# Performance work log

Measured on AMD Instinct MI355X. Metric: run time of the kernel, lower is better.

The kernel has to match this reference:

```python
import jax, jax.numpy as jnp
import numpy as np
from jax.scipy.linalg import solve_triangular

EPS = 2e-05  # module eps (original only adds it on Cholesky failure)
NUM_LABELS = 8


def setup_inputs() -> dict:
    key = jax.random.key(0)
    k1, k2, k3, k4 = jax.random.split(key, 4)
    B, N, H, W = 1, 256, 512, 512
    return {
        "content_feat": jax.random.normal(k1, (B, N, H, W), dtype=jnp.float32),
        "style_feat": jax.random.normal(k2, (B, N, H, W), dtype=jnp.float32),
        "content_seg": jax.random.randint(k3, (H, W), 0, NUM_LABELS, dtype=jnp.int32),
        "style_seg": jax.random.randint(k4, (H, W), 0, NUM_LABELS, dtype=jnp.int32),
        "num_labels": NUM_LABELS,
    }


def _cwct(c, s, seg_c, seg_s, num_labels):
    # c, s: (N, M) flattened features; seg_*: (M,) int labels
    N = c.shape[0]
    eye = jnp.eye(N, dtype=c.dtype)
    target = c
    for l in range(num_labels):  # fixed small label count
        mc = (seg_c == l)  # (Mc,) content mask
        ms = (seg_s == l)
        nc = mc.sum().astype(c.dtype)
        ns = ms.sum().astype(c.dtype)
        nc1 = jnp.maximum(nc, 1.0)
        ns1 = jnp.maximum(ns, 1.0)
        # masked mean + centered (zeros outside mask)
        mean_c = (c * mc).sum(-1) / nc1
        xc = (c - mean_c[:, None]) * mc  # (N, M)
        cov_c = (xc @ xc.T) / jnp.maximum(nc1 - 1.0, 1.0)  # (N, N)
        Lc = jnp.linalg.cholesky(cov_c)
        inv_Lc = solve_triangular(Lc, eye, lower=True)
        white = inv_Lc @ xc
        # style stats + coloring
        mean_s = (s * ms).sum(-1) / ns1
        xs = (s - mean_s[:, None]) * ms
        cov_s = (xs @ xs.T) / jnp.maximum(ns1 - 1.0, 1.0)
        Ls = jnp.linalg.cholesky(cov_s)
        colored = Ls @ white + mean_s[:, None]
        # label validity: >10 pixels each side, count ratio < 100
        valid = (nc > 10) & (ns > 10) & (nc < 100.0 * ns) & (ns < 100.0 * nc)
        target = jnp.where(mc[None, :] & valid, colored, target)
    return target


def reference(content_feat, style_feat, content_seg, style_seg, num_labels):
    B, N, cH, cW = content_feat.shape  # B == 1 (original code only supports B=1)
    c = content_feat.reshape(N, cH * cW)
    s = style_feat.reshape(N, -1)
    out = _cwct(c, s, content_seg.reshape(-1), style_seg.reshape(-1), num_labels)
    return out.reshape(B, N, cH, cW)
```

## Files before the change

kernel.cpp:

```cpp
#include <hip/hip_runtime.h>

#define NCH   256
#define M_PIX 262144
#define MPAD  266240
#define LDA   40

typedef short bf16x8 __attribute__((ext_vector_type(8)));
typedef float f32x4  __attribute__((ext_vector_type(4)));

__device__ __forceinline__ unsigned short f2bf(float f) {
  union { float f; unsigned u; } v; v.f = f;
  unsigned r = v.u + 0x7FFFu + ((v.u >> 16) & 1u);
  return (unsigned short)(r >> 16);
}
__device__ __forceinline__ float bf2f(unsigned short h) {
  union { unsigned u; float f; } v; v.u = ((unsigned)h) << 16;
  return v.f;
}

__global__ __launch_bounds__(256) void k_hist(const int* __restrict__ seg_c,
                                              const int* __restrict__ seg_s,
                                              int* __restrict__ hist) {
  __shared__ int h[16];
  int t = threadIdx.x;
  if (t < 16) h[t] = 0;
  __syncthreads();
  int p0 = blockIdx.x * 2048 + t * 8;
#pragma unroll
  for (int e = 0; e < 8; ++e) {
    atomicAdd(&h[seg_c[p0 + e] & 7], 1);
    atomicAdd(&h[8 + (seg_s[p0 + e] & 7)], 1);
  }
  __syncthreads();
  if (t < 8) hist[blockIdx.x * 8 + t] = h[t];
  else if (t < 16) hist[1024 + blockIdx.x * 8 + (t - 8)] = h[t];
}

__global__ __launch_bounds__(256) void k_scan(const int* __restrict__ hist,
                                              int* __restrict__ base,
                                              int* __restrict__ off,
                                              int* __restrict__ cnt,
                                              int* __restrict__ valid) {
  __shared__ int lh[2048];
  __shared__ int tot[16];
  __shared__ int loff[2][9];
  int t = threadIdx.x;
  for (int i = t; i < 2048; i += 256) lh[i] = hist[i];
  __syncthreads();
  if (t < 16) {
    int s = t >> 3, l = t & 7, acc = 0;
    for (int b = 0; b < 128; ++b) acc += lh[s * 1024 + b * 8 + l];
    tot[t] = acc;
  }
  __syncthreads();
  if (t < 2) {
    int run = 0;
    for (int l = 0; l < 8; ++l) {
      loff[t][l] = run;
      run = (run + tot[t * 8 + l] + 511) & ~511;
    }
    loff[t][8] = run;
    for (int l = 0; l < 9; ++l) off[t * 9 + l] = loff[t][l];
    for (int l = 0; l < 8; ++l) cnt[t * 8 + l] = tot[t * 8 + l];
  }
  __syncthreads();
  if (t < 8) {
    long nc = tot[t], ns = tot[8 + t];
    valid[t] = (nc > 10 && ns > 10 && nc < 100 * ns && ns < 100 * nc) ? 1 : 0;
  }
  if (t < 16) {
    int s = t >> 3, l = t & 7;
    int run = loff[s][l];
    for (int b = 0; b < 128; ++b) {
      base[s * 1024 + b * 8 + l] = run;
      run += lh[s * 1024 + b * 8 + l];
    }
  }
}

__global__ __launch_bounds__(256) void k_rank(const int* __restrict__ seg_c,
                                              const int* __restrict__ seg_s,
                                              const int* __restrict__ base,
                                              int* __restrict__ dst) {
  __shared__ int sc[8 * 272];
  __shared__ int rb[256 * 8];
  __shared__ int bb[8];
  int t = threadIdx.x;
  for (int s = 0; s < 2; ++s) {
    const int* seg = s ? seg_s : seg_c;
    const int* bas = base + s * 1024 + blockIdx.x * 8;
    int* dd = dst + (size_t)s * M_PIX;
    int p0 = blockIdx.x * 2048 + t * 8;
    unsigned pk2 = 0, cpk = 0;
#pragma unroll
    for (int e = 0; e < 8; ++e) {
      int lb = seg[p0 + e] & 7;
      pk2 |= (unsigned)lb << (3 * e);
      cpk += 1u << (4 * lb);
    }
#pragma unroll
    for (int lq = 0; lq < 8; ++lq) sc[lq * 272 + t] = (int)((cpk >> (4 * lq)) & 15u);
    if (t < 8) bb[t] = bas[t];
    __syncthreads();
    for (int d = 1; d < 256; d <<= 1) {
      int v[8];
#pragma unroll
      for (int lq = 0; lq < 8; ++lq)
        v[lq] = sc[lq * 272 + t] + ((t >= d) ? sc[lq * 272 + t - d] : 0);
      __syncthreads();
#pragma unroll
      for (int lq = 0; lq < 8; ++lq) sc[lq * 272 + t] = v[lq];
      __syncthreads();
    }
#pragma unroll
    for (int lq = 0; lq < 8; ++lq)
      rb[t * 8 + lq] = bb[lq] + sc[lq * 272 + t] - (int)((cpk >> (4 * lq)) & 15u);
#pragma unroll
    for (int e = 0; e < 8; ++e) {
      int lb = (int)((pk2 >> (3 * e)) & 7u);
      int dpos = rb[t * 8 + lb]++;
      dd[p0 + e] = dpos;
    }
    __syncthreads();
  }
}

__global__ __launch_bounds__(256) void k_padzero(unsigned short* __restrict__ P,
                                                 const int* __restrict__ off,
                                                 const int* __restrict__ cnt) {
  int l = blockIdx.x;
  int c0, c1;
  if (l < 8) { c0 = off[l] + cnt[l]; c1 = off[l + 1]; }
  else       { c0 = off[8];          c1 = MPAD; }
  int w = c1 - c0;
  if (w <= 0) return;
  for (int r = 0; r < 256; ++r)
    for (int cc = threadIdx.x; cc < w; cc += 256)
      P[(size_t)r * MPAD + c0 + cc] = 0;
}

__global__ __launch_bounds__(256) void k_pack(const float* __restrict__ feat,
                                              const int* __restrict__ seg,
                                              const int* __restrict__ dst,
                                              const int* __restrict__ base,
                                              unsigned short* __restrict__ P) {
  int b = blockIdx.x, g = blockIdx.y, t = threadIdx.x;
  int p0 = b * 2048;
  __shared__ unsigned short buf[8][2048];
  __shared__ int h[8], lbase[9], gbase[8];
  if (t < 8) { h[t] = 0; gbase[t] = base[b * 8 + t]; }
  __syncthreads();
  int lbr[2][4], slotr[2][4], gd[8];
#pragma unroll
  for (int j = 0; j < 2; ++j) {
    int4 sg = *(const int4*)&seg[p0 + j * 1024 + t * 4];
    lbr[j][0] = sg.x & 7; lbr[j][1] = sg.y & 7;
    lbr[j][2] = sg.z & 7; lbr[j][3] = sg.w & 7;
#pragma unroll
    for (int e = 0; e < 4; ++e) atomicAdd(&h[lbr[j][e]], 1);
  }
  __syncthreads();
  if (t == 0) {
    int run = 0;
    for (int l = 0; l < 8; ++l) { lbase[l] = run; run += h[l]; }
    lbase[8] = run;
  }
  __syncthreads();
#pragma unroll
  for (int j = 0; j < 2; ++j) {
    int4 dv = *(const int4*)&dst[p0 + j * 1024 + t * 4];
    slotr[j][0] = lbase[lbr[j][0]] + (dv.x - gbase[lbr[j][0]]);
    slotr[j][1] = lbase[lbr[j][1]] + (dv.y - gbase[lbr[j][1]]);
    slotr[j][2] = lbase[lbr[j][2]] + (dv.z - gbase[lbr[j][2]]);
    slotr[j][3] = lbase[lbr[j][3]] + (dv.w - gbase[lbr[j][3]]);
  }
#pragma unroll
  for (int i = 0; i < 8; ++i) {
    int q = i * 256 + t;
    int l = 0;
    while (l < 7 && q >= lbase[l + 1]) ++l;
    gd[i] = gbase[l] + q - lbase[l];
  }
  int n0 = g * 32;
#pragma unroll 1
  for (int cp = 0; cp < 4; ++cp) {
#pragma unroll
    for (int c = 0; c < 8; ++c) {
      const float* fp = &feat[(size_t)(n0 + cp * 8 + c) * M_PIX + p0];
      float4 v0 = *(const float4*)&fp[t * 4];
      float4 v1 = *(const float4*)&fp[1024 + t * 4];
      buf[c][slotr[0][0]] = f2bf(v0.x); buf[c][slotr[0][1]] = f2bf(v0.y);
      buf[c][slotr[0][2]] = f2bf(v0.z); buf[c][slotr[0][3]] = f2bf(v0.w);
      buf[c][slotr[1][0]] = f2bf(v1.x); buf[c][slotr[1][1]] = f2bf(v1.y);
      buf[c][slotr[1][2]] = f2bf(v1.z); buf[c][slotr[1][3]] = f2bf(v1.w);
    }
    __syncthreads();
#pragma unroll
    for (int c = 0; c < 8; ++c) {
      unsigned short* pp = &P[(size_t)(n0 + cp * 8 + c) * MPAD];
#pragma unroll
      for (int i = 0; i < 8; ++i)
        pp[gd[i]] = buf[c][i * 256 + t];
    }
    __syncthreads();
  }
}

__global__ __launch_bounds__(256) void k_unpack(const unsigned short* __restrict__ P,
                                                const int* __restrict__ seg,
                                                const int* __restrict__ dst,
                                                const int* __restrict__ base,
                                                float* __restrict__ out) {
  int b = blockIdx.x, g = blockIdx.y, t = threadIdx.x;
  int p0 = b * 2048;
  __shared__ unsigned short buf[8][2048];
  __shared__ int h[8], lbase[9], gbase[8];
  if (t < 8) { h[t] = 0; gbase[t] = base[b * 8 + t]; }
  __syncthreads();
  int lbr[2][4], slotr[2][4], gd[8];
#pragma unroll
  for (int j = 0; j < 2; ++j) {
    int4 sg = *(const int4*)&seg[p0 + j * 1024 + t * 4];
    lbr[j][0] = sg.x & 7; lbr[j][1] = sg.y & 7;
    lbr[j][2] = sg.z & 7; lbr[j][3] = sg.w & 7;
#pragma unroll
    for (int e = 0; e < 4; ++e) atomicAdd(&h[lbr[j][e]], 1);
  }
  __syncthreads();
  if (t == 0) {
    int run = 0;
    for (int l = 0; l < 8; ++l) { lbase[l] = run; run += h[l]; }
    lbase[8] = run;
  }
  __syncthreads();
#pragma unroll
  for (int j = 0; j < 2; ++j) {
    int4 dv = *(const int4*)&dst[p0 + j * 1024 + t * 4];
    slotr[j][0] = lbase[lbr[j][0]] + (dv.x - gbase[lbr[j][0]]);
    slotr[j][1] = lbase[lbr[j][1]] + (dv.y - gbase[lbr[j][1]]);
    slotr[j][2] = lbase[lbr[j][2]] + (dv.z - gbase[lbr[j][2]]);
    slotr[j][3] = lbase[lbr[j][3]] + (dv.w - gbase[lbr[j][3]]);
  }
#pragma unroll
  for (int i = 0; i < 8; ++i) {
    int q = i * 256 + t;
    int l = 0;
    while (l < 7 && q >= lbase[l + 1]) ++l;
    gd[i] = gbase[l] + q - lbase[l];
  }
  int n0 = g * 32;
#pragma unroll 1
  for (int cp = 0; cp < 4; ++cp) {
#pragma unroll
    for (int c = 0; c < 8; ++c) {
      const unsigned short* pp = &P[(size_t)(n0 + cp * 8 + c) * MPAD];
#pragma unroll
      for (int i = 0; i < 8; ++i)
        buf[c][i * 256 + t] = pp[gd[i]];
    }
    __syncthreads();
#pragma unroll
    for (int c = 0; c < 8; ++c) {
      float* op = &out[(size_t)(n0 + cp * 8 + c) * M_PIX + p0];
      float4 v0, v1;
      v0.x = bf2f(buf[c][slotr[0][0]]); v0.y = bf2f(buf[c][slotr[0][1]]);
      v0.z = bf2f(buf[c][slotr[0][2]]); v0.w = bf2f(buf[c][slotr[0][3]]);
      v1.x = bf2f(buf[c][slotr[1][0]]); v1.y = bf2f(buf[c][slotr[1][1]]);
      v1.z = bf2f(buf[c][slotr[1][2]]); v1.w = bf2f(buf[c][slotr[1][3]]);
      *(float4*)&op[t * 4] = v0;
      *(float4*)&op[1024 + t * 4] = v1;
    }
    __syncthreads();
  }
}

__global__ __launch_bounds__(512) void k_gram(const unsigned short* __restrict__ P,
                                              const int* __restrict__ off,
                                              float* __restrict__ G,
                                              float* __restrict__ sum) {
  int l = blockIdx.y;
  long o0 = off[l], o1 = off[l + 1];
  long k0 = o0 + (long)blockIdx.x * 1024;
  if (k0 >= o1) return;
  long rem = o1 - k0;
  int ks = rem > 1024 ? 1024 : (int)rem;

  __shared__ unsigned short Sb[256 * LDA];
  int t = threadIdx.x, wave = t >> 6, lane = t & 63;
  int wr = (wave < 2) ? wave * 64 : 128 + (wave & 1) * 64;
  int wc = (wave >= 4) ? 128 : 0;
  bool wact = (wave < 6);

  f32x4 acc[4][8] = {};
  float rsum = 0.0f;

  for (int kk = 0; kk < ks; kk += 32) {
#pragma unroll
    for (int it = 0; it < 2; ++it) {
      int slot = t + it * 512;
      int rr = slot >> 2, gg = slot & 3;
      *(uint4*)&Sb[rr * LDA + gg * 8] =
          *(const uint4*)&P[(size_t)rr * MPAD + (size_t)(k0 + kk) + gg * 8];
    }
    __syncthreads();
    if (t < 256) {
#pragma unroll
      for (int e = 0; e < 16; ++e) {
        unsigned v = *(const unsigned*)&Sb[t * LDA + e * 2];
        rsum += bf2f((unsigned short)(v & 0xFFFFu)) + bf2f((unsigned short)(v >> 16));
      }
    }
    if (wact) {
      bf16x8 bfr[8];
#pragma unroll
      for (int fj = 0; fj < 8; ++fj)
        bfr[fj] = *(const bf16x8*)&Sb[(wc + fj * 16 + (lane & 15)) * LDA + (lane >> 4) * 8];
#pragma unroll
      for (int fi = 0; fi < 4; ++fi) {
        bf16x8 afr = *(const bf16x8*)&Sb[(wr + fi * 16 + (lane & 15)) * LDA + (lane >> 4) * 8];
#pragma unroll
        for (int fj = 0; fj < 8; ++fj)
          acc[fi][fj] = __builtin_amdgcn_mfma_f32_16x16x32_bf16(afr, bfr[fj], acc[fi][fj], 0, 0, 0);
      }
    }
    __syncthreads();
  }
  float* Gl = G + ((size_t)l << 16);
  if (wact) {
#pragma unroll
    for (int fi = 0; fi < 4; ++fi)
#pragma unroll
      for (int fj = 0; fj < 8; ++fj) {
        int cc = wc + fj * 16 + (lane & 15);
#pragma unroll
        for (int rg = 0; rg < 4; ++rg) {
          int rr2 = wr + fi * 16 + (lane >> 4) * 4 + rg;
          atomicAdd(&Gl[rr2 * 256 + cc], acc[fi][fj][rg]);
        }
      }
  }
  if (t < 256) atomicAdd(&sum[l * 256 + t], rsum);
}

__global__ __launch_bounds__(256) void k_cov(float* __restrict__ G,
                                             const float* __restrict__ sum,
                                             const int* __restrict__ cnt,
                                             float* __restrict__ means,
                                             float* __restrict__ bacc) {
  int bid = blockIdx.x;
  float* A = G + ((size_t)bid << 16);
  int t = threadIdx.x;
  __shared__ float mu[256];
  float fc = (float)cnt[bid];
  float m = sum[bid * 256 + t] / fmaxf(fc, 1.0f);
  mu[t] = m;
  means[bid * 256 + t] = m;
  if (bid >= 8) bacc[(bid - 8) * 256 + t] = m;
  __syncthreads();
  float rdiv = 1.0f / fmaxf(fmaxf(fc, 1.0f) - 1.0f, 1.0f);
  float mt = mu[t];
  for (int i = t; i < 256; ++i) {
    float g = A[i * 256 + t];
    A[t * 256 + i] = (g - fc * mu[i] * mt) * rdiv;
  }
}

__global__ __launch_bounds__(256) void k_panel64(float* __restrict__ G,
                                                 float* __restrict__ Wg, int pb) {
  float* LT = G + ((size_t)blockIdx.x << 16);
  int t = threadIdx.x;
  int jb = pb * 64;
  int nT = 224 - jb;
  __shared__ float W1[32 * 36];
  __shared__ float W2[32 * 36];
  __shared__ float Cb[32][33];
  __shared__ float Db[32][33];

  if (t < 64) {
    int l32 = t & 31;
    float x[32];
#pragma unroll
    for (int k = 0; k < 32; ++k)
      x[k] = (k <= l32) ? LT[(size_t)(jb + k) * 256 + jb + l32] : 0.0f;
#pragma unroll
    for (int j = 0; j < 32; ++j) {
      float dj = __shfl(x[j], j, 64);
      float rd = 1.0f / sqrtf(dj);
      float lj = x[j] * rd;
      x[j] = lj;
#pragma unroll
      for (int k = j + 1; k < 32; ++k)
        x[k] -= lj * __shfl(lj, k, 64);
    }
    if (t < 32) {
#pragma unroll
      for (int k = 0; k < 32; ++k)
        if (k <= l32) LT[(size_t)(jb + k) * 256 + jb + l32] = x[k];
    }
    float w[32];
#pragma unroll
    for (int k = 0; k < 32; ++k) w[k] = 0.0f;
#pragma unroll
    for (int i2 = 0; i2 < 32; ++i2) {
      float s = (i2 == l32) ? 1.0f : 0.0f;
#pragma unroll
      for (int k = 0; k < 32; ++k)
        if (k < i2) s -= __shfl(x[k], i2, 64) * w[k];
      float wv = s / __shfl(x[i2], i2, 64);
      w[i2] = (i2 >= l32) ? wv : 0.0f;
    }
    if (t < 32) {
      float* Wgp = Wg + (((size_t)blockIdx.x * 8 + 2 * pb) << 10);
#pragma unroll
      for (int i2 = 0; i2 < 32; ++i2)
        if (i2 >= l32) { W1[i2 * 36 + l32] = w[i2]; Wgp[i2 * 32 + l32] = w[i2]; }
    }
  }
  __syncthreads();

  float xx[32], bb[32];
  if (t < nT) {
    int row = jb + 32 + t;
    float a[32];
#pragma unroll
    for (int k = 0; k < 32; ++k) a[k] = LT[(size_t)(jb + k) * 256 + row];
#pragma unroll
    for (int j = 0; j < 32; ++j) {
      float s = 0.0f;
#pragma unroll
      for (int k = 0; k < 32; ++k)
        if (k <= j) s += a[k] * W1[j * 36 + k];
      xx[j] = s;
      LT[(size_t)(jb + j) * 256 + row] = s;
    }
    if (t < 32) {
#pragma unroll
      for (int j = 0; j < 32; ++j) Cb[t][j] = xx[j];
    }
  }
  __syncthreads();

  if (t < nT) {
    int row = jb + 32 + t;
#pragma unroll
    for (int c = 0; c < 32; ++c) {
      float s = LT[(size_t)(jb + 32 + c) * 256 + row];
#pragma unroll
      for (int k = 0; k < 32; ++k) s -= xx[k] * Cb[c][k];
      bb[c] = s;
    }
    if (t < 32) {
#pragma unroll
      for (int c = 0; c < 32; ++c) Db[t][c] = bb[c];
    }
  }
  __syncthreads();

  if (t < 64) {
    int l32 = t & 31;
    float x[32];
#pragma unroll
    for (int k = 0; k < 32; ++k) x[k] = (k <= l32) ? Db[l32][k] : 0.0f;
#pragma unroll
    for (int j = 0; j < 32; ++j) {
      float dj = __shfl(x[j], j, 64);
      float rd = 1.0f / sqrtf(dj);
      float lj = x[j] * rd;
      x[j] = lj;
#pragma unroll
      for (int k = j + 1; k < 32; ++k)
        x[k] -= lj * __shfl(lj, k, 64);
    }
    if (t < 32) {
#pragma unroll
      for (int k = 0; k < 32; ++k)
        if (k <= l32) LT[(size_t)(jb + 32 + k) * 256 + jb + 32 + l32] = x[k];
    }
    float w[32];
#pragma unroll
    for (int k = 0; k < 32; ++k) w[k] = 0.0f;
#pragma unroll
    for (int i2 = 0; i2 < 32; ++i2) {
      float s = (i2 == l32) ? 1.0f : 0.0f;
#pragma unroll
      for (int k = 0; k < 32; ++k)
        if (k < i2) s -= __shfl(x[k], i2, 64) * w[k];
      float wv = s / __shfl(x[i2], i2, 64);
      w[i2] = (i2 >= l32) ? wv : 0.0f;
    }
    if (t < 32) {
      float* Wgp = Wg + (((size_t)blockIdx.x * 8 + 2 * pb + 1) << 10);
#pragma unroll
      for (int i2 = 0; i2 < 32; ++i2)
        if (i2 >= l32) { W2[i2 * 36 + l32] = w[i2]; Wgp[i2 * 32 + l32] = w[i2]; }
    }
  }
  __syncthreads();

  if (t >= 32 && t < nT) {
    int row = jb + 32 + t;
#pragma unroll
    for (int j = 0; j < 32; ++j) {
      float s = 0.0f;
#pragma unroll
      for (int k = 0; k < 32; ++k)
        if (k <= j) s += bb[k] * W2[j * 36 + k];
      LT[(size_t)(jb + 32 + j) * 256 + row] = s;
    }
  }
}

__global__ __launch_bounds__(256) void k_trail64(float* __restrict__ G, int pb) {
  int jb = pb * 64;
  int H2 = 192 - jb;
  int nts2 = H2 >> 6;
  int y = blockIdx.y;
  if (y >= (nts2 * (nts2 + 1)) >> 1) return;
  int ti = 0;
  while ((((ti + 1) * (ti + 2)) >> 1) <= y) ++ti;
  int tj = y - ((ti * (ti + 1)) >> 1);
  float* LT = G + ((size_t)blockIdx.x << 16);
  int i0 = jb + 64 + ti * 64, j0 = jb + 64 + tj * 64;

  __shared__ float Li[64][64];
  __shared__ float Lj[64][64];
  int t = threadIdx.x;
  for (int idx = t; idx < 4096; idx += 256) {
    int k = idx >> 6, r = idx & 63;
    Li[k][r] = LT[(size_t)(jb + k) * 256 + i0 + r];
    Lj[k][r] = LT[(size_t)(jb + k) * 256 + j0 + r];
  }
  __syncthreads();

  int tx = t & 15, ty = t >> 4;
  float acc[4][4] = {};
#pragma unroll 4
  for (int k = 0; k < 64; ++k) {
    float4 a = *(const float4*)&Li[k][ty * 4];
    float4 b = *(const float4*)&Lj[k][tx * 4];
    acc[0][0] += a.x * b.x; acc[0][1] += a.x * b.y; acc[0][2] += a.x * b.z; acc[0][3] += a.x * b.w;
    acc[1][0] += a.y * b.x; acc[1][1] += a.y * b.y; acc[1][2] += a.y * b.z; acc[1][3] += a.y * b.w;
    acc[2][0] += a.z * b.x; acc[2][1] += a.z * b.y; acc[2][2] += a.z * b.z; acc[2][3] += a.z * b.w;
    acc[3][0] += a.w * b.x; acc[3][1] += a.w * b.y; acc[3][2] += a.w * b.z; acc[3][3] += a.w * b.w;
  }
#pragma unroll
  for (int jj = 0; jj < 4; ++jj) {
    int j = j0 + tx * 4 + jj;
    float* col = &LT[(size_t)j * 256 + i0 + ty * 4];
#pragma unroll
    for (int ii = 0; ii < 4; ++ii) {
      int i = i0 + ty * 4 + ii;
      if (i >= j) col[ii] -= acc[ii][jj];
    }
  }
}

__global__ __launch_bounds__(256) void k_vlevel32w(const float* __restrict__ G,
                                                   const float* __restrict__ Wg,
                                                   float* __restrict__ Vinv) {
  int l = blockIdx.x >> 2, pair = blockIdx.x & 3;
  const float* LT = G + ((size_t)l << 16);
  float* V = Vinv + ((size_t)l << 16);
  const float* W1g = Wg + (((size_t)l * 8 + 2 * pair) << 10);
  const float* W2g = Wg + (((size_t)l * 8 + 2 * pair + 1) << 10);
  int d = pair * 64;
  int t = threadIdx.x;
  __shared__ float A[32][33];
  __shared__ float B[32][33];
  __shared__ float C[32][33];
  for (int idx = t; idx < 1024; idx += 256) {
    int i = idx >> 5, j = idx & 31;
    A[i][j] = LT[(size_t)(d + j) * 256 + d + 32 + i];
    float w1 = (i >= j) ? W1g[idx] : 0.0f;
    B[i][j] = w1;
    V[(size_t)(d + i) * 256 + d + j] = w1;
  }
  __syncthreads();
  for (int idx = t; idx < 1024; idx += 256) {
    int i = idx >> 5, j = idx & 31;
    float s = 0.0f;
#pragma unroll
    for (int k = 0; k < 32; ++k) s += A[i][k] * B[k][j];
    C[i][j] = s;
  }
  __syncthreads();
  for (int idx = t; idx < 1024; idx += 256) {
    int i = idx >> 5, j = idx & 31;
    float w2 = (i >= j) ? W2g[idx] : 0.0f;
    B[i][j] = w2;
    V[(size_t)(d + 32 + i) * 256 + d + 32 + j] = w2;
  }
  __syncthreads();
  for (int idx = t; idx < 1024; idx += 256) {
    int i = idx >> 5, j = idx & 31;
    float s = 0.0f;
#pragma unroll
    for (int k = 0; k < 32; ++k) s += B[i][k] * C[k][j];
    V[(size_t)(d + 32 + i) * 256 + d + j] = -s;
  }
}

template <int N>
__global__ __launch_bounds__(512) void k_vlevel(const float* __restrict__ G,
                                                float* __restrict__ Vinv) {
  constexpr int NP = 256 / (2 * N);
  constexpr int RPT = N / 32;
  constexpr int CPT = N / 16;
  int unit = blockIdx.x;
  int l = unit / NP, pair = unit % NP;
  const float* LT = G + ((size_t)l << 16);
  float* V = Vinv + ((size_t)l << 16);
  int d = pair * 2 * N;
  int t = threadIdx.x;
  int cg = t & 15, rg = t >> 4;
  int r0 = rg * RPT, c0 = cg * CPT;

  __shared__ float Abuf[N][N + 4];
  __shared__ float Bbuf[N][N + 4];

  for (int idx = t; idx < N * N; idx += 512) {
    int k = idx / N, r = idx % N;
    Abuf[r][k] = LT[(size_t)(d + k) * 256 + d + N + r];
  }
  for (int idx = t; idx < N * N; idx += 512) {
    int k = idx / N, c = idx % N;
    Bbuf[k][c] = V[(size_t)(d + k) * 256 + d + c];
  }
  __syncthreads();

  float acc[RPT][CPT];
#pragma unroll
  for (int i = 0; i < RPT; ++i)
#pragma unroll
    for (int j = 0; j < CPT; ++j) acc[i][j] = 0.0f;
  for (int k = 0; k < N; ++k) {
    float av[RPT];
#pragma unroll
    for (int i = 0; i < RPT; ++i) av[i] = Abuf[r0 + i][k];
#pragma unroll
    for (int j = 0; j < CPT; ++j) {
      float bv = Bbuf[k][c0 + j];
#pragma unroll
      for (int i = 0; i < RPT; ++i) acc[i][j] += av[i] * bv;
    }
  }
  __syncthreads();
#pragma unroll
  for (int i = 0; i < RPT; ++i)
#pragma unroll
    for (int j = 0; j < CPT; ++j) Abuf[r0 + i][c0 + j] = acc[i][j];
  for (int idx = t; idx < N * N; idx += 512) {
    int r = idx / N, k = idx % N;
    Bbuf[r][k] = V[(size_t)(d + N + r) * 256 + d + N + k];
  }
  __syncthreads();

#pragma unroll
  for (int i = 0; i < RPT; ++i)
#pragma unroll
    for (int j = 0; j < CPT; ++j) acc[i][j] = 0.0f;
  for (int k = 0; k < N; ++k) {
    float av[RPT];
#pragma unroll
    for (int i = 0; i < RPT; ++i) av[i] = Bbuf[r0 + i][k];
#pragma unroll
    for (int j = 0; j < CPT; ++j) {
      float bv = Abuf[k][c0 + j];
#pragma unroll
      for (int i = 0; i < RPT; ++i) acc[i][j] += av[i] * bv;
    }
  }
#pragma unroll
  for (int i = 0; i < RPT; ++i)
#pragma unroll
    for (int j = 0; j < CPT; ++j)
      V[(size_t)(d + N + r0 + i) * 256 + d + c0 + j] = -acc[i][j];
}

__global__ __launch_bounds__(256) void k_tgemm(const float* __restrict__ G,
                                               const float* __restrict__ Vinv,
                                               const float* __restrict__ means,
                                               const int* __restrict__ valid,
                                               unsigned short* __restrict__ Tb,
                                               float* __restrict__ bacc) {
  int l = blockIdx.y;
  int ti = blockIdx.x >> 2, tj = blockIdx.x & 3;
  unsigned short* Tbl = Tb + ((size_t)l << 16);
  int i0 = ti * 64, j0 = tj * 64;
  int t = threadIdx.x;
  if (!valid[l]) {
    if (tj == 0 && t < 64) bacc[l * 256 + i0 + t] = 0.0f;
    for (int idx = t; idx < 4096; idx += 256) {
      int i = idx >> 6, j = idx & 63;
      Tbl[(size_t)(i0 + i) * 256 + j0 + j] = f2bf((i0 + i) == (j0 + j) ? 1.0f : 0.0f);
    }
    return;
  }
  if (tj > ti) {
    for (int idx = t; idx < 4096; idx += 256) {
      int i = idx >> 6, j = idx & 63;
      Tbl[(size_t)(i0 + i) * 256 + j0 + j] = 0;
    }
    return;
  }
  const float* LTs = G + ((size_t)(8 + l) << 16);
  const float* V = Vinv + ((size_t)l << 16);

  __shared__ float As[64][260];
  __shared__ __align__(16) float Bs[256][68];

  for (int idx = t; idx < 64 * 256; idx += 256) {
    int k = idx >> 6, i = idx & 63;
    As[i][k] = (i0 + i >= k) ? LTs[(size_t)k * 256 + i0 + i] : 0.0f;
  }
  for (int idx = t; idx < 64 * 256; idx += 256) {
    int k = idx >> 6, j = idx & 63;
    Bs[k][j] = V[(size_t)k * 256 + j0 + j];
  }
  __syncthreads();

  int tx = t & 15, ty = t >> 4;
  float acc[4][4] = {};
  int klo = j0, khi = i0 + 64;
  for (int k = klo; k < khi; ++k) {
    float a0 = As[ty * 4 + 0][k], a1 = As[ty * 4 + 1][k];
    float a2 = As[ty * 4 + 2][k], a3 = As[ty * 4 + 3][k];
    float4 b = *(const float4*)&Bs[k][tx * 4];
    acc[0][0] += a0 * b.x; acc[0][1] += a0 * b.y; acc[0][2] += a0 * b.z; acc[0][3] += a0 * b.w;
    acc[1][0] += a1 * b.x; acc[1][1] += a1 * b.y; acc[1][2] += a1 * b.z; acc[1][3] += a1 * b.w;
    acc[2][0] += a2 * b.x; acc[2][1] += a2 * b.y; acc[2][2] += a2 * b.z; acc[2][3] += a2 * b.w;
    acc[3][0] += a3 * b.x; acc[3][1] += a3 * b.y; acc[3][2] += a3 * b.z; acc[3][3] += a3 * b.w;
  }
  float mc[4];
#pragma unroll
  for (int cc = 0; cc < 4; ++cc) mc[cc] = means[l * 256 + j0 + tx * 4 + cc];
#pragma unroll
  for (int rr = 0; rr < 4; ++rr) {
    int i = i0 + ty * 4 + rr;
    float partial = 0.0f;
#pragma unroll
    for (int cc = 0; cc < 4; ++cc) {
      Tbl[(size_t)i * 256 + j0 + tx * 4 + cc] = f2bf(acc[rr][cc]);
      partial += acc[rr][cc] * mc[cc];
    }
    atomicAdd(&bacc[l * 256 + i], -partial);
  }
}

__global__ __launch_bounds__(512) void k_outgemm(unsigned short* __restrict__ P,
                                                 const unsigned short* __restrict__ Tb,
                                                 const float* __restrict__ bvec,
                                                 const int* __restrict__ off) {
  long px0 = (long)blockIdx.x * 256;
  if (px0 >= off[8]) return;
  int l = 0;
  while (l < 7 && px0 >= off[l + 1]) ++l;
  const unsigned short* Tl = Tb + ((size_t)l << 16);

  __shared__ unsigned short As[256 * LDA];
  __shared__ unsigned short Bs[256 * LDA];
  __shared__ float bsh[256];

  int t = threadIdx.x, wave = t >> 6, lane = t & 63;
  int wrow = (wave & 3) * 64;
  int ph = wave >> 2;
  if (t < 256) bsh[t] = bvec[l * 256 + t];

  f32x4 acc[4][8] = {};

  for (int kk = 0; kk < 256; kk += 32) {
#pragma unroll
    for (int it = 0; it < 2; ++it) {
      int slot = t + it * 512;
      int rr = slot >> 2, gg = slot & 3;
      *(uint4*)&As[rr * LDA + gg * 8] = *(const uint4*)&Tl[rr * 256 + kk + gg * 8];
    }
#pragma unroll
    for (int it = 0; it < 2; ++it) {
      int slot = t + it * 512;
      int pg = slot & 31, kr = slot >> 5;
      uint4 v = *(const uint4*)&P[(size_t)(kk + kr) * MPAD + px0 + pg * 8];
      const unsigned short* vs = (const unsigned short*)&v;
      int krs = kr ^ ((pg & 3) << 3);
#pragma unroll
      for (int e = 0; e < 8; ++e) Bs[(pg * 8 + e) * LDA + krs] = vs[e];
    }
    __syncthreads();
    if (kk < wrow + 64) {
      bf16x8 bfr[8];
#pragma unroll
      for (int fj = 0; fj < 8; ++fj) {
        int px = ph * 128 + fj * 16 + (lane & 15);
        int gs = (lane >> 4) ^ ((px >> 3) & 3);
        bfr[fj] = *(const bf16x8*)&Bs[px * LDA + gs * 8];
      }
#pragma unroll
      for (int fi = 0; fi < 4; ++fi) {
        if (wrow + fi * 16 + 15 >= kk) {
          bf16x8 afr = *(const bf16x8*)&As[(wrow + fi * 16 + (lane & 15)) * LDA + (lane >> 4) * 8];
#pragma unroll
          for (int fj = 0; fj < 8; ++fj)
            acc[fi][fj] = __builtin_amdgcn_mfma_f32_16x16x32_bf16(afr, bfr[fj], acc[fi][fj], 0, 0, 0);
        }
      }
    }
    __syncthreads();
  }
#pragma unroll
  for (int fi = 0; fi < 4; ++fi)
#pragma unroll
    for (int fj = 0; fj < 8; ++fj) {
      long p = px0 + ph * 128 + fj * 16 + (lane & 15);
#pragma unroll
      for (int rg = 0; rg < 4; ++rg) {
        int rr = wrow + fi * 16 + (lane >> 4) * 4 + rg;
        float v = acc[fi][fj][rg] + bsh[rr];
        P[(size_t)rr * MPAD + p] = f2bf(v);
      }
    }
}

extern "C" void kernel_launch(void* const* d_in, const int* in_sizes, int n_in,
                              void* d_out, int out_size, void* d_ws, size_t ws_size,
                              hipStream_t stream) {
  const float* cfeat = (const float*)d_in[0];
  const float* sfeat = (const float*)d_in[1];
  const int* seg_c   = (const int*)d_in[2];
  const int* seg_s   = (const int*)d_in[3];

  char* ws = (char*)d_ws;
  size_t o = 0;
  auto take = [&](size_t b) { size_t r = o; o += (b + 255) & ~(size_t)255; return r; };

  unsigned short* P  = (unsigned short*)(ws + take((size_t)NCH * MPAD * 2));
  size_t zero_b = o;
  float* G           = (float*)(ws + take((size_t)2 * 8 * 65536 * 4));
  float* Vinv        = (float*)(ws + take((size_t)8 * 65536 * 4));
  float* sum         = (float*)(ws + take((size_t)2 * 8 * 256 * 4));
  float* bacc        = (float*)(ws + take((size_t)8 * 256 * 4));
  int*   hist        = (int*)(ws + take((size_t)2 * 128 * 8 * 4));
  size_t zero_e = o;
  unsigned short* Tb = (unsigned short*)(ws + take((size_t)8 * 65536 * 2));
  float* Wg          = (float*)(ws + take((size_t)16 * 8 * 1024 * 4));
  int*   dst         = (int*)(ws + take((size_t)2 * M_PIX * 4));
  float* means       = (float*)(ws + take((size_t)2 * 8 * 256 * 4));
  int*   base        = (int*)(ws + take((size_t)2 * 128 * 8 * 4));
  int*   off         = (int*)(ws + take((size_t)2 * 9 * 4));
  int*   cnt         = (int*)(ws + take((size_t)2 * 8 * 4));
  int*   valid       = (int*)(ws + take((size_t)8 * 4));
  (void)ws_size; (void)n_in; (void)in_sizes; (void)out_size;

  hipMemsetAsync(ws + zero_b, 0, zero_e - zero_b, stream);

  k_hist<<<dim3(128), dim3(256), 0, stream>>>(seg_c, seg_s, hist);
  k_scan<<<dim3(1), dim3(256), 0, stream>>>(hist, base, off, cnt, valid);
  k_rank<<<dim3(128), dim3(256), 0, stream>>>(seg_c, seg_s, base, dst);

  for (int s = 1; s >= 0; --s) {
    const float* feat = s ? sfeat : cfeat;
    const int* seg = s ? seg_s : seg_c;
    k_padzero<<<dim3(9), dim3(256), 0, stream>>>(P, off + s * 9, cnt + s * 8);
    k_pack<<<dim3(128, 8), dim3(256), 0, stream>>>(feat, seg, dst + (size_t)s * M_PIX,
                                                   base + s * 1024, P);
    k_gram<<<dim3(260, 8), dim3(512), 0, stream>>>(P, off + s * 9, G + (size_t)s * 8 * 65536,
                                                   sum + (size_t)s * 8 * 256);
  }

  k_cov<<<dim3(16), dim3(256), 0, stream>>>(G, sum, cnt, means, bacc);
  for (int pb = 0; pb < 4; ++pb) {
    k_panel64<<<dim3(16), dim3(256), 0, stream>>>(G, Wg, pb);
    if (pb < 3) {
      int nts2 = (192 - 64 * pb) >> 6;
      k_trail64<<<dim3(16, (nts2 * (nts2 + 1)) >> 1), dim3(256), 0, stream>>>(G, pb);
    }
  }
  k_vlevel32w<<<dim3(32), dim3(256), 0, stream>>>(G, Wg, Vinv);
  k_vlevel<64><<<dim3(16), dim3(512), 0, stream>>>(G, Vinv);
  k_vlevel<128><<<dim3(8), dim3(512), 0, stream>>>(G, Vinv);
  k_tgemm<<<dim3(16, 8), dim3(256), 0, stream>>>(G, Vinv, means, valid, Tb, bacc);
  k_outgemm<<<dim3(1040), dim3(512), 0, stream>>>(P, Tb, bacc, off);
  k_unpack<<<dim3(128, 8), dim3(256), 0, stream>>>(P, seg_c, dst, base, (float*)d_out);
}
```

Measured before the change: 1.145 ms.

## Split Gram kernel into 128x128 quadrant blocks and parallelize pad zeroing

The Gram kernel is retiled so that each 256-thread block computes one of three 128x128 quadrants (the lower-triangle blocks of the symmetric 256x256 Gram) over a 512-pixel K slice, instead of 512-thread blocks where two of eight waves sat idle. Rows not needed for a quadrant are no longer loaded into LDS, and the row-sum work is assigned to the diagonal-free quadrant. The aim is more blocks, better occupancy, and no idle waves, at the cost of reloading each row panel across quadrants and issuing more atomics. The pad-zero kernel is split across 16 row groups to add parallelism. The outgemm row index also changes, and this looks like a fix or an equivalent rewrite.

```diff
diff --git a/kernel.cpp b/kernel.cpp
--- a/kernel.cpp
+++ b/kernel.cpp
@@ -134,7 +134,8 @@
   else       { c0 = off[8];          c1 = MPAD; }
   int w = c1 - c0;
   if (w <= 0) return;
-  for (int r = 0; r < 256; ++r)
+  int r0 = blockIdx.y * 16;
+  for (int r = r0; r < r0 + 16; ++r)
     for (int cc = threadIdx.x; cc < w; cc += 256)
       P[(size_t)r * MPAD + c0 + cc] = 0;
 }
@@ -274,72 +275,77 @@
   }
 }
 
-__global__ __launch_bounds__(512) void k_gram(const unsigned short* __restrict__ P,
+__global__ __launch_bounds__(256) void k_gram(const unsigned short* __restrict__ P,
                                               const int* __restrict__ off,
                                               float* __restrict__ G,
                                               float* __restrict__ sum) {
   int l = blockIdx.y;
   long o0 = off[l], o1 = off[l + 1];
-  long k0 = o0 + (long)blockIdx.x * 1024;
+  long k0 = o0 + (long)blockIdx.x * 512;
   if (k0 >= o1) return;
-  long rem = o1 - k0;
-  int ks = rem > 1024 ? 1024 : (int)rem;
-
-  __shared__ unsigned short Sb[256 * LDA];
-  int t = threadIdx.x, wave = t >> 6, lane = t & 63;
-  int wr = (wave < 2) ? wave * 64 : 128 + (wave & 1) * 64;
-  int wc = (wave >= 4) ? 128 : 0;
-  bool wact = (wave < 6);
-
-  f32x4 acc[4][8] = {};
+  int qz = blockIdx.z;
+  int qi = (qz == 0) ? 0 : 1;
+  int qj = (qz == 2) ? 1 : 0;
+
+  __shared__ unsigned short As[128 * LDA];
+  __shared__ unsigned short Bs[128 * LDA];
+
+  int t = threadIdx.x;
+  int wave = t >> 6, lane = t & 63;
+  int wr = (wave >> 1) * 64, wc = (wave & 1) * 64;
+
+  f32x4 acc[4][4] = {};
   float rsum = 0.0f;
 
-  for (int kk = 0; kk < ks; kk += 32) {
+  for (int kk = 0; kk < 512; kk += 32) {
 #pragma unroll
     for (int it = 0; it < 2; ++it) {
-      int slot = t + it * 512;
+      int slot = t + it * 256;
       int rr = slot >> 2, gg = slot & 3;
-      *(uint4*)&Sb[rr * LDA + gg * 8] =
-          *(const uint4*)&P[(size_t)rr * MPAD + (size_t)(k0 + kk) + gg * 8];
-    }
-    __syncthreads();
-    if (t < 256) {
+      *(uint4*)&As[rr * LDA + gg * 8] =
+          *(const uint4*)&P[(size_t)(qi * 128 + rr) * MPAD + (size_t)(k0 + kk) + gg * 8];
+      *(uint4*)&Bs[rr * LDA + gg * 8] =
+          *(const uint4*)&P[(size_t)(qj * 128 + rr) * MPAD + (size_t)(k0 + kk) + gg * 8];
+    }
+    __syncthreads();
+    if (qz == 1) {
+      const unsigned short* src = (t < 128) ? &As[t * LDA] : &Bs[(t - 128) * LDA];
 #pragma unroll
       for (int e = 0; e < 16; ++e) {
-        unsigned v = *(const unsigned*)&Sb[t * LDA + e * 2];
+        unsigned v = *(const unsigned*)&src[e * 2];
         rsum += bf2f((unsigned short)(v & 0xFFFFu)) + bf2f((unsigned short)(v >> 16));
       }
     }
-    if (wact) {
-      bf16x8 bfr[8];
-#pragma unroll
-      for (int fj = 0; fj < 8; ++fj)
-        bfr[fj] = *(const bf16x8*)&Sb[(wc + fj * 16 + (lane & 15)) * LDA + (lane >> 4) * 8];
-#pragma unroll
-      for (int fi = 0; fi < 4; ++fi) {
-        bf16x8 afr = *(const bf16x8*)&Sb[(wr + fi * 16 + (lane & 15)) * LDA + (lane >> 4) * 8];
-#pragma unroll
-        for (int fj = 0; fj < 8; ++fj)
-          acc[fi][fj] = __builtin_amdgcn_mfma_f32_16x16x32_bf16(afr, bfr[fj], acc[fi][fj], 0, 0, 0);
+    bf16x8 bfr[4];
+#pragma unroll
+    for (int fj = 0; fj < 4; ++fj)
+      bfr[fj] = *(const bf16x8*)&Bs[(wc + fj * 16 + (lane & 15)) * LDA + (lane >> 4) * 8];
+#pragma unroll
+    for (int fi = 0; fi < 4; ++fi) {
+      bf16x8 afr = *(const bf16x8*)&As[(wr + fi * 16 + (lane & 15)) * LDA + (lane >> 4) * 8];
+#pragma unroll
+      for (int fj = 0; fj < 4; ++fj)
+        acc[fi][fj] = __builtin_amdgcn_mfma_f32_16x16x32_bf16(afr, bfr[fj], acc[fi][fj], 0, 0, 0);
+    }
+    __syncthreads();
+  }
+  float* Gl = G + ((size_t)l << 16);
+  int rb = qi * 128 + wr, cb = qj * 128 + wc;
+#pragma unroll
+  for (int fi = 0; fi < 4; ++fi)
+#pragma unroll
+    for (int fj = 0; fj < 4; ++fj) {
+      int cc = cb + fj * 16 + (lane & 15);
+#pragma unroll
+      for (int rg = 0; rg < 4; ++rg) {
+        int rr = rb + fi * 16 + (lane >> 4) * 4 + rg;
+        atomicAdd(&Gl[rr * 256 + cc], acc[fi][fj][rg]);
       }
     }
-    __syncthreads();
-  }
-  float* Gl = G + ((size_t)l << 16);
-  if (wact) {
-#pragma unroll
-    for (int fi = 0; fi < 4; ++fi)
-#pragma unroll
-      for (int fj = 0; fj < 8; ++fj) {
-        int cc = wc + fj * 16 + (lane & 15);
-#pragma unroll
-        for (int rg = 0; rg < 4; ++rg) {
-          int rr2 = wr + fi * 16 + (lane >> 4) * 4 + rg;
-          atomicAdd(&Gl[rr2 * 256 + cc], acc[fi][fj][rg]);
-        }
-      }
-  }
-  if (t < 256) atomicAdd(&sum[l * 256 + t], rsum);
+  if (qz == 1) {
+    int row = (t < 128) ? (128 + t) : (t - 128);
+    atomicAdd(&sum[l * 256 + row], rsum);
+  }
 }
 
 __global__ __launch_bounds__(256) void k_cov(float* __restrict__ G,
@@ -813,7 +819,7 @@
       long p = px0 + ph * 128 + fj * 16 + (lane & 15);
 #pragma unroll
       for (int rg = 0; rg < 4; ++rg) {
-        int rr = wrow + fi * 16 + (lane >> 4) * 4 + rg;
+        int rr = (wave & 3) * 64 + fi * 16 + (lane >> 4) * 4 + rg;
         float v = acc[fi][fj][rg] + bsh[rr];
         P[(size_t)rr * MPAD + p] = f2bf(v);
       }
@@ -859,11 +865,12 @@
   for (int s = 1; s >= 0; --s) {
     const float* feat = s ? sfeat : cfeat;
     const int* seg = s ? seg_s : seg_c;
-    k_padzero<<<dim3(9), dim3(256), 0, stream>>>(P, off + s * 9, cnt + s * 8);
+    k_padzero<<<dim3(9, 16), dim3(256), 0, stream>>>(P, off + s * 9, cnt + s * 8);
     k_pack<<<dim3(128, 8), dim3(256), 0, stream>>>(feat, seg, dst + (size_t)s * M_PIX,
                                                    base + s * 1024, P);
-    k_gram<<<dim3(260, 8), dim3(512), 0, stream>>>(P, off + s * 9, G + (size_t)s * 8 * 65536,
-                                                   sum + (size_t)s * 8 * 256);
+    k_gram<<<dim3(520, 8, 3), dim3(256), 0, stream>>>(P, off + s * 9,
+                                                      G + (size_t)s * 8 * 65536,
+                                                      sum + (size_t)s * 8 * 256);
   }
 
   k_cov<<<dim3(16), dim3(256), 0, stream>>>(G, sum, cnt, means, bacc);
```

Result: faster. 1.078 ms (-5.8%).
